# Kernel optimization log

Measured on AMD Instinct MI355X. Metric: run time of the kernel, lower is better.

Reference implementation:

```python
import jax, jax.numpy as jnp
import numpy as np

P, R = 8, 8            # mlp_quad_last_shape: (P, rank)
N, D_IN, HID = 32768, 3, 1024
NQ, QD, QHID = 64, 1, 128


def _mlp2(x, Wa, ba, Wb, bb):
    # two-layer MLP with tanh, matches a standard DecGreenNet MLP block
    return jnp.tanh(x @ Wa + ba) @ Wb + bb


def setup_inputs() -> dict:
    key = jax.random.key(0)
    ks = jax.random.split(key, 32)
    sn = lambda k, shape, scale: (jax.random.normal(k, shape, jnp.float32) * scale)
    inp = {
        "input": jax.random.normal(ks[0], (N, D_IN), jnp.float32),
        "eq_param": jnp.ones((1,), jnp.float32),
        "W1": sn(ks[1], (D_IN, HID), 1.0 / np.sqrt(D_IN)),
        "b1": jnp.zeros((HID,), jnp.float32),
        "W2": sn(ks[2], (HID, P ** 4), 1.0 / np.sqrt(HID)),
        "b2": jnp.zeros((P ** 4,), jnp.float32),
    }
    for i in range(4):
        inp[f"quad_x{i}"] = jax.random.uniform(ks[3 + i], (NQ, QD), jnp.float32)
        inp[f"Wq{i}a"] = sn(ks[7 + 2 * i], (QD, QHID), 1.0)
        inp[f"bq{i}a"] = jnp.zeros((QHID,), jnp.float32)
        inp[f"Wq{i}b"] = sn(ks[8 + 2 * i], (QHID, P * R), 1.0 / np.sqrt(QHID))
        inp[f"bq{i}b"] = jnp.zeros((P * R,), jnp.float32)
    return inp


def reference(input, eq_param, W1, b1, W2, b2,
              quad_x0, quad_x1, quad_x2, quad_x3,
              Wq0a, bq0a, Wq0b, bq0b,
              Wq1a, bq1a, Wq1b, bq1b,
              Wq2a, bq2a, Wq2b, bq2b,
              Wq3a, bq3a, Wq3b, bq3b):
    # lhs = mlp_x(input): [N, P^4]
    lhs = _mlp2(input, W1, b1, W2, b2)

    quads = [(quad_x0, Wq0a, bq0a, Wq0b, bq0b),
             (quad_x1, Wq1a, bq1a, Wq1b, bq1b),
             (quad_x2, Wq2a, bq2a, Wq2b, bq2b),
             (quad_x3, Wq3a, bq3a, Wq3b, bq3b)]

    # Per-factor: y_i * mlp_quad_i(quad_x_i), reshape to [n_i, P, R], sum over quad points.
    # Summing the 8-D outer product over its four quadrature axes factorizes exactly
    # into these per-factor sums S_i followed by a rank contraction (same math as
    # the torch einsum+movedim+reshape+sum, without the (n*P)^4 intermediate).
    Ss = []
    for qx, Wa, ba, Wb, bb in quads:
        y = eq_param * jnp.prod(jnp.sin(jnp.pi * qx), axis=-1, keepdims=True)  # [n,1]
        oq = (y * _mlp2(qx, Wa, ba, Wb, bb)).reshape(-1, P, R)                 # [n,P,R]
        Ss.append(oq.sum(axis=0))                                              # [P,R]

    # rhs[b,d,f,m] = sum_x S0[b,x] S1[d,x] S2[f,x] S3[m,x]; flatten in (b,d,f,m) order
    rhs = jnp.einsum('bx,dx,fx,mx->bdfm', *Ss).reshape(-1)  # [P^4]
    return lhs @ rhs  # [N]
```

## Files before the change

### kernel.cpp

```cpp
#include <hip/hip_runtime.h>
#include <math.h>

#define HID   1024
#define P4    4096

__device__ __forceinline__ float fast_tanh(float x) {
    float e = __expf(-2.0f * fabsf(x));
    float t = (1.0f - e) * __builtin_amdgcn_rcpf(1.0f + e);
    return copysignf(t, x);
}

__global__ __launch_bounds__(256) void k_factors_rhs(
    const float* __restrict__ eq,
    const float* __restrict__ qx0, const float* __restrict__ wa0, const float* __restrict__ ba0,
    const float* __restrict__ wb0, const float* __restrict__ bb0,
    const float* __restrict__ qx1, const float* __restrict__ wa1, const float* __restrict__ ba1,
    const float* __restrict__ wb1, const float* __restrict__ bb1,
    const float* __restrict__ qx2, const float* __restrict__ wa2, const float* __restrict__ ba2,
    const float* __restrict__ wb2, const float* __restrict__ bb2,
    const float* __restrict__ qx3, const float* __restrict__ wa3, const float* __restrict__ ba3,
    const float* __restrict__ wb3, const float* __restrict__ bb3,
    const float* __restrict__ b2,
    float* __restrict__ rhs, float* __restrict__ b2r)
{
    __shared__ float2 qy_s[4][64];
    __shared__ float  wh_s[4][128];
    __shared__ float  S_s[4][64];
    __shared__ float  red[256];

    const int t    = threadIdx.x;
    const int lane = t & 63;
    const int f    = t >> 6;

    const float* qx; const float* wa; const float* ba; const float* wb; const float* bb;
    if (f == 0)      { qx = qx0; wa = wa0; ba = ba0; wb = wb0; bb = bb0; }
    else if (f == 1) { qx = qx1; wa = wa1; ba = ba1; wb = wb1; bb = bb1; }
    else if (f == 2) { qx = qx2; wa = wa2; ba = ba2; wb = wb2; bb = bb2; }
    else             { qx = qx3; wa = wa3; ba = ba3; wb = wb3; bb = bb3; }

    const float qv = qx[lane];
    const float yv = eq[0] * sinf((float)M_PI * qv);
    qy_s[f][lane] = make_float2(qv, yv);

    float ysum = yv;
    #pragma unroll
    for (int off = 32; off; off >>= 1) ysum += __shfl_xor(ysum, off);

    __syncthreads();

    {
        const float w0 = wa[lane],      c0 = ba[lane];
        const float w1 = wa[lane + 64], c1 = ba[lane + 64];
        float a0 = 0.f, a1 = 0.f;
        #pragma unroll 8
        for (int p = 0; p < 64; ++p) {
            float2 qy = qy_s[f][p];
            a0 += qy.y * fast_tanh(fmaf(qy.x, w0, c0));
            a1 += qy.y * fast_tanh(fmaf(qy.x, w1, c1));
        }
        wh_s[f][lane]      = a0;
        wh_s[f][lane + 64] = a1;
    }
    __syncthreads();

    {
        float acc = bb[lane] * ysum;
        #pragma unroll 8
        for (int h = 0; h < 128; ++h)
            acc = fmaf(wh_s[f][h], wb[h * 64 + lane], acc);
        S_s[f][lane] = acc;
    }
    __syncthreads();

    float local = 0.f;
    for (int i = t; i < P4; i += 256) {
        const int m  = i & 7;
        const int fq = (i >> 3) & 7;
        const int d  = (i >> 6) & 7;
        const int b  = (i >> 9) & 7;
        float acc = 0.f;
        #pragma unroll
        for (int x = 0; x < 8; ++x)
            acc += S_s[0][b * 8 + x] * S_s[1][d * 8 + x]
                 * S_s[2][fq * 8 + x] * S_s[3][m * 8 + x];
        rhs[i] = acc;
        local = fmaf(b2[i], acc, local);
    }

    red[t] = local;
    __syncthreads();
    if (t < 128) red[t] += red[t + 128];
    __syncthreads();
    if (t < 64) {
        float v = red[t] + red[t + 64];
        #pragma unroll
        for (int off = 32; off; off >>= 1) v += __shfl_xor(v, off);
        if (t == 0) b2r[0] = v;
    }
}

__global__ __launch_bounds__(256) void k_w2r(
    const float* __restrict__ W2, const float* __restrict__ rhs,
    float* __restrict__ w2r)
{
    const int wave = threadIdx.x >> 6;
    const int lane = threadIdx.x & 63;
    const int row  = blockIdx.x * 4 + wave;

    const float4* w4 = (const float4*)(W2 + (size_t)row * P4);
    const float4* r4 = (const float4*)rhs;

    float acc = 0.f;
    #pragma unroll
    for (int i = 0; i < 16; ++i) {
        const int k = lane + 64 * i;
        float4 a = w4[k];
        float4 b = r4[k];
        acc += a.x * b.x + a.y * b.y + a.z * b.z + a.w * b.w;
    }
    #pragma unroll
    for (int off = 32; off; off >>= 1) acc += __shfl_down(acc, off);
    if (lane == 0) w2r[row] = acc;
}

__global__ __launch_bounds__(256) void k_out(
    const float* __restrict__ input,
    const float* __restrict__ W1, const float* __restrict__ b1,
    const float* __restrict__ w2r, const float* __restrict__ b2r,
    float* __restrict__ out)
{
    __shared__ float4 wpack[HID];
    __shared__ float  w2rs[HID];
    __shared__ float  part[4][64];

    const int t = threadIdx.x;
    #pragma unroll
    for (int h = t; h < HID; h += 256) {
        wpack[h] = make_float4(W1[h], W1[HID + h], W1[2 * HID + h], b1[h]);
        w2rs[h]  = w2r[h];
    }
    __syncthreads();

    const int lane = t & 63;
    const int wave = t >> 6;
    const int row  = blockIdx.x * 64 + lane;
    const float* x = input + (size_t)row * 3;
    const float x0 = x[0], x1 = x[1], x2 = x[2];

    float acc = 0.f;
    const int h0 = wave * 256;
    #pragma unroll 8
    for (int h = h0; h < h0 + 256; ++h) {
        float4 wp = wpack[h];
        float pre = fmaf(x0, wp.x, fmaf(x1, wp.y, fmaf(x2, wp.z, wp.w)));
        acc = fmaf(fast_tanh(pre), w2rs[h], acc);
    }

    part[wave][lane] = acc;
    __syncthreads();
    if (t < 64)
        out[blockIdx.x * 64 + t] =
            part[0][t] + part[1][t] + part[2][t] + part[3][t] + b2r[0];
}

extern "C" void kernel_launch(void* const* d_in, const int* in_sizes, int n_in,
                              void* d_out, int out_size, void* d_ws, size_t ws_size,
                              hipStream_t stream)
{
    const float* input = (const float*)d_in[0];
    const float* eq    = (const float*)d_in[1];
    const float* W1    = (const float*)d_in[2];
    const float* b1    = (const float*)d_in[3];
    const float* W2    = (const float*)d_in[4];
    const float* b2    = (const float*)d_in[5];
    const float* q[4][5];
    for (int i = 0; i < 4; ++i)
        for (int k = 0; k < 5; ++k)
            q[i][k] = (const float*)d_in[6 + 5 * i + k];

    float* ws  = (float*)d_ws;
    float* rhs = ws;
    float* w2r = ws + 4096;
    float* b2r = ws + 5120;
    float* out = (float*)d_out;

    hipLaunchKernelGGL(k_factors_rhs, dim3(1), dim3(256), 0, stream,
        eq,
        q[0][0], q[0][1], q[0][2], q[0][3], q[0][4],
        q[1][0], q[1][1], q[1][2], q[1][3], q[1][4],
        q[2][0], q[2][1], q[2][2], q[2][3], q[2][4],
        q[3][0], q[3][1], q[3][2], q[3][3], q[3][4],
        b2, rhs, b2r);

    hipLaunchKernelGGL(k_w2r, dim3(256), dim3(256), 0, stream,
        W2, rhs, w2r);

    hipLaunchKernelGGL(k_out, dim3(512), dim3(256), 0, stream,
        input, W1, b1, w2r, b2r, out);
}
```

Measured before the change: 143.8 us.

## Fuse three kernels into one cooperative kernel with grid syncs and prefetched W2

Replaces the three launches (factor/rhs, W2·rhs, output MLP) with a single cooperative kernel of 1024 blocks that uses grid.sync between phases. Each block loads its W2 row into registers before the first sync, hiding that load behind the single-block factor computation. Each block then recomputes the full rhs vector in shared memory instead of reading it from global memory. This removes launch gaps and the serialized single-block stage, at the cost of grid-wide barrier overhead, redundant rhs computation, and a requirement that all 1024 blocks be co-resident.

```diff
diff --git a/kernel.cpp b/kernel.cpp
--- a/kernel.cpp
+++ b/kernel.cpp
@@ -1,8 +1,22 @@
 #include <hip/hip_runtime.h>
+#include <hip/hip_cooperative_groups.h>
 #include <math.h>
 
-#define HID   1024
-#define P4    4096
+#define HID 1024
+#define P4  4096
+
+namespace cg = cooperative_groups;
+
+struct Params {
+    const float* input; const float* eq;
+    const float* W1; const float* b1; const float* W2; const float* b2;
+    const float* qx[4]; const float* wa[4]; const float* ba[4];
+    const float* wb[4]; const float* bb[4];
+    float* Sg;
+    float* w2r;
+    float* b2r;
+    float* out;
+};
 
 __device__ __forceinline__ float fast_tanh(float x) {
     float e = __expf(-2.0f * fabsf(x));
@@ -10,70 +24,71 @@
     return copysignf(t, x);
 }
 
-__global__ __launch_bounds__(256) void k_factors_rhs(
-    const float* __restrict__ eq,
-    const float* __restrict__ qx0, const float* __restrict__ wa0, const float* __restrict__ ba0,
-    const float* __restrict__ wb0, const float* __restrict__ bb0,
-    const float* __restrict__ qx1, const float* __restrict__ wa1, const float* __restrict__ ba1,
-    const float* __restrict__ wb1, const float* __restrict__ bb1,
-    const float* __restrict__ qx2, const float* __restrict__ wa2, const float* __restrict__ ba2,
-    const float* __restrict__ wb2, const float* __restrict__ bb2,
-    const float* __restrict__ qx3, const float* __restrict__ wa3, const float* __restrict__ ba3,
-    const float* __restrict__ wb3, const float* __restrict__ bb3,
-    const float* __restrict__ b2,
-    float* __restrict__ rhs, float* __restrict__ b2r)
+__global__ __launch_bounds__(256, 4) void k_fused(Params p)
 {
-    __shared__ float2 qy_s[4][64];
-    __shared__ float  wh_s[4][128];
-    __shared__ float  S_s[4][64];
-    __shared__ float  red[256];
+    union SharedU {
+        struct { float2 qy[64]; float wh[128]; } a;
+        struct { float S[256]; float rhs[P4]; float red[256]; } b;
+        struct { float4 wpack[HID]; float w2rs[HID]; float part[8][32]; } c;
+    };
+    __shared__ SharedU sm;
 
-    const int t    = threadIdx.x;
-    const int lane = t & 63;
-    const int f    = t >> 6;
+    cg::grid_group grid = cg::this_grid();
+    const int bid = blockIdx.x;
+    const int t   = threadIdx.x;
 
-    const float* qx; const float* wa; const float* ba; const float* wb; const float* bb;
-    if (f == 0)      { qx = qx0; wa = wa0; ba = ba0; wb = wb0; bb = bb0; }
-    else if (f == 1) { qx = qx1; wa = wa1; ba = ba1; wb = wb1; bb = bb1; }
-    else if (f == 2) { qx = qx2; wa = wa2; ba = ba2; wb = wb2; bb = bb2; }
-    else             { qx = qx3; wa = wa3; ba = ba3; wb = wb3; bb = bb3; }
+    float4 wreg0, wreg1, wreg2, wreg3;
+    {
+        const float4* w4 = (const float4*)(p.W2 + (size_t)bid * P4);
+        wreg0 = w4[t];
+        wreg1 = w4[t + 256];
+        wreg2 = w4[t + 512];
+        wreg3 = w4[t + 768];
+    }
 
-    const float qv = qx[lane];
-    const float yv = eq[0] * sinf((float)M_PI * qv);
-    qy_s[f][lane] = make_float2(qv, yv);
+    if (bid < 4) {
+        const float* qx = p.qx[bid]; const float* wa = p.wa[bid];
+        const float* ba = p.ba[bid]; const float* wb = p.wb[bid];
+        const float* bb = p.bb[bid];
 
-    float ysum = yv;
-    #pragma unroll
-    for (int off = 32; off; off >>= 1) ysum += __shfl_xor(ysum, off);
+        float ysum = 0.f;
+        if (t < 64) {
+            float qv = qx[t];
+            float yv = p.eq[0] * sinf((float)M_PI * qv);
+            sm.a.qy[t] = make_float2(qv, yv);
+            ysum = yv;
+            #pragma unroll
+            for (int off = 32; off; off >>= 1) ysum += __shfl_xor(ysum, off);
+        }
+        __syncthreads();
+        if (t < 128) {
+            float w = wa[t], c0 = ba[t], a = 0.f;
+            #pragma unroll 8
+            for (int q = 0; q < 64; ++q) {
+                float2 qy = sm.a.qy[q];
+                a += qy.y * fast_tanh(fmaf(qy.x, w, c0));
+            }
+            sm.a.wh[t] = a;
+        }
+        __syncthreads();
+        if (t < 64) {
+            float acc = bb[t] * ysum;
+            #pragma unroll 8
+            for (int h = 0; h < 128; ++h)
+                acc = fmaf(sm.a.wh[h], wb[h * 64 + t], acc);
+            p.Sg[bid * 64 + t] = acc;
+        }
+    }
 
+    grid.sync();
+
+    sm.b.S[t] = p.Sg[t];
     __syncthreads();
 
-    {
-        const float w0 = wa[lane],      c0 = ba[lane];
-        const float w1 = wa[lane + 64], c1 = ba[lane + 64];
-        float a0 = 0.f, a1 = 0.f;
-        #pragma unroll 8
-        for (int p = 0; p < 64; ++p) {
-            float2 qy = qy_s[f][p];
-            a0 += qy.y * fast_tanh(fmaf(qy.x, w0, c0));
-            a1 += qy.y * fast_tanh(fmaf(qy.x, w1, c1));
-        }
-        wh_s[f][lane]      = a0;
-        wh_s[f][lane + 64] = a1;
-    }
-    __syncthreads();
-
-    {
-        float acc = bb[lane] * ysum;
-        #pragma unroll 8
-        for (int h = 0; h < 128; ++h)
-            acc = fmaf(wh_s[f][h], wb[h * 64 + lane], acc);
-        S_s[f][lane] = acc;
-    }
-    __syncthreads();
-
-    float local = 0.f;
-    for (int i = t; i < P4; i += 256) {
+    float b2local = 0.f;
+    #pragma unroll
+    for (int k = 0; k < 16; ++k) {
+        const int i = t + 256 * k;
         const int m  = i & 7;
         const int fq = (i >> 3) & 7;
         const int d  = (i >> 6) & 7;
@@ -81,120 +96,99 @@
         float acc = 0.f;
         #pragma unroll
         for (int x = 0; x < 8; ++x)
-            acc += S_s[0][b * 8 + x] * S_s[1][d * 8 + x]
-                 * S_s[2][fq * 8 + x] * S_s[3][m * 8 + x];
-        rhs[i] = acc;
-        local = fmaf(b2[i], acc, local);
-    }
-
-    red[t] = local;
-    __syncthreads();
-    if (t < 128) red[t] += red[t + 128];
-    __syncthreads();
-    if (t < 64) {
-        float v = red[t] + red[t + 64];
-        #pragma unroll
-        for (int off = 32; off; off >>= 1) v += __shfl_xor(v, off);
-        if (t == 0) b2r[0] = v;
-    }
-}
-
-__global__ __launch_bounds__(256) void k_w2r(
-    const float* __restrict__ W2, const float* __restrict__ rhs,
-    float* __restrict__ w2r)
-{
-    const int wave = threadIdx.x >> 6;
-    const int lane = threadIdx.x & 63;
-    const int row  = blockIdx.x * 4 + wave;
-
-    const float4* w4 = (const float4*)(W2 + (size_t)row * P4);
-    const float4* r4 = (const float4*)rhs;
-
-    float acc = 0.f;
-    #pragma unroll
-    for (int i = 0; i < 16; ++i) {
-        const int k = lane + 64 * i;
-        float4 a = w4[k];
-        float4 b = r4[k];
-        acc += a.x * b.x + a.y * b.y + a.z * b.z + a.w * b.w;
-    }
-    #pragma unroll
-    for (int off = 32; off; off >>= 1) acc += __shfl_down(acc, off);
-    if (lane == 0) w2r[row] = acc;
-}
-
-__global__ __launch_bounds__(256) void k_out(
-    const float* __restrict__ input,
-    const float* __restrict__ W1, const float* __restrict__ b1,
-    const float* __restrict__ w2r, const float* __restrict__ b2r,
-    float* __restrict__ out)
-{
-    __shared__ float4 wpack[HID];
-    __shared__ float  w2rs[HID];
-    __shared__ float  part[4][64];
-
-    const int t = threadIdx.x;
-    #pragma unroll
-    for (int h = t; h < HID; h += 256) {
-        wpack[h] = make_float4(W1[h], W1[HID + h], W1[2 * HID + h], b1[h]);
-        w2rs[h]  = w2r[h];
+            acc += sm.b.S[b * 8 + x]       * sm.b.S[64 + d * 8 + x]
+                 * sm.b.S[128 + fq * 8 + x] * sm.b.S[192 + m * 8 + x];
+        sm.b.rhs[i] = acc;
+        if (bid == 0) b2local = fmaf(p.b2[i], acc, b2local);
     }
     __syncthreads();
 
-    const int lane = t & 63;
-    const int wave = t >> 6;
-    const int row  = blockIdx.x * 64 + lane;
-    const float* x = input + (size_t)row * 3;
+    {
+        const float4* r4 = (const float4*)sm.b.rhs;
+        float4 a0 = r4[t], a1 = r4[t + 256], a2 = r4[t + 512], a3 = r4[t + 768];
+        float acc = wreg0.x * a0.x + wreg0.y * a0.y + wreg0.z * a0.z + wreg0.w * a0.w
+                  + wreg1.x * a1.x + wreg1.y * a1.y + wreg1.z * a1.z + wreg1.w * a1.w
+                  + wreg2.x * a2.x + wreg2.y * a2.y + wreg2.z * a2.z + wreg2.w * a2.w
+                  + wreg3.x * a3.x + wreg3.y * a3.y + wreg3.z * a3.z + wreg3.w * a3.w;
+        sm.b.red[t] = acc;
+    }
+    __syncthreads();
+    if (t < 64) {
+        float v = sm.b.red[t] + sm.b.red[t + 64] + sm.b.red[t + 128] + sm.b.red[t + 192];
+        #pragma unroll
+        for (int off = 32; off; off >>= 1) v += __shfl_xor(v, off);
+        if (t == 0) p.w2r[bid] = v;
+    }
+    if (bid == 0) {
+        __syncthreads();
+        sm.b.red[t] = b2local;
+        __syncthreads();
+        if (t < 64) {
+            float v = sm.b.red[t] + sm.b.red[t + 64] + sm.b.red[t + 128] + sm.b.red[t + 192];
+            #pragma unroll
+            for (int off = 32; off; off >>= 1) v += __shfl_xor(v, off);
+            if (t == 0) p.b2r[0] = v;
+        }
+    }
+
+    grid.sync();
+
+    #pragma unroll
+    for (int h = t; h < HID; h += 256) {
+        sm.c.wpack[h] = make_float4(p.W1[h], p.W1[HID + h], p.W1[2 * HID + h], p.b1[h]);
+        sm.c.w2rs[h]  = p.w2r[h];
+    }
+    __syncthreads();
+
+    const int r = t & 31;
+    const int c = t >> 5;
+    const int row = bid * 32 + r;
+    const float* x = p.input + (size_t)row * 3;
     const float x0 = x[0], x1 = x[1], x2 = x[2];
 
     float acc = 0.f;
-    const int h0 = wave * 256;
+    const int h0 = c * 128;
     #pragma unroll 8
-    for (int h = h0; h < h0 + 256; ++h) {
-        float4 wp = wpack[h];
+    for (int h = h0; h < h0 + 128; ++h) {
+        float4 wp = sm.c.wpack[h];
         float pre = fmaf(x0, wp.x, fmaf(x1, wp.y, fmaf(x2, wp.z, wp.w)));
-        acc = fmaf(fast_tanh(pre), w2rs[h], acc);
+        acc = fmaf(fast_tanh(pre), sm.c.w2rs[h], acc);
     }
-
-    part[wave][lane] = acc;
+    sm.c.part[c][r] = acc;
     __syncthreads();
-    if (t < 64)
-        out[blockIdx.x * 64 + t] =
-            part[0][t] + part[1][t] + part[2][t] + part[3][t] + b2r[0];
+    if (t < 32) {
+        float v = p.b2r[0];
+        #pragma unroll
+        for (int cc = 0; cc < 8; ++cc) v += sm.c.part[cc][t];
+        p.out[bid * 32 + t] = v;
+    }
 }
 
 extern "C" void kernel_launch(void* const* d_in, const int* in_sizes, int n_in,
                               void* d_out, int out_size, void* d_ws, size_t ws_size,
                               hipStream_t stream)
 {
-    const float* input = (const float*)d_in[0];
-    const float* eq    = (const float*)d_in[1];
-    const float* W1    = (const float*)d_in[2];
-    const float* b1    = (const float*)d_in[3];
-    const float* W2    = (const float*)d_in[4];
-    const float* b2    = (const float*)d_in[5];
-    const float* q[4][5];
-    for (int i = 0; i < 4; ++i)
-        for (int k = 0; k < 5; ++k)
-            q[i][k] = (const float*)d_in[6 + 5 * i + k];
+    Params p;
+    p.input = (const float*)d_in[0];
+    p.eq    = (const float*)d_in[1];
+    p.W1    = (const float*)d_in[2];
+    p.b1    = (const float*)d_in[3];
+    p.W2    = (const float*)d_in[4];
+    p.b2    = (const float*)d_in[5];
+    for (int i = 0; i < 4; ++i) {
+        p.qx[i] = (const float*)d_in[6 + 5 * i + 0];
+        p.wa[i] = (const float*)d_in[6 + 5 * i + 1];
+        p.ba[i] = (const float*)d_in[6 + 5 * i + 2];
+        p.wb[i] = (const float*)d_in[6 + 5 * i + 3];
+        p.bb[i] = (const float*)d_in[6 + 5 * i + 4];
+    }
+    float* ws = (float*)d_ws;
+    p.Sg  = ws;
+    p.w2r = ws + 256;
+    p.b2r = ws + 1280;
+    p.out = (float*)d_out;
 
-    float* ws  = (float*)d_ws;
-    float* rhs = ws;
-    float* w2r = ws + 4096;
-    float* b2r = ws + 5120;
-    float* out = (float*)d_out;
-
-    hipLaunchKernelGGL(k_factors_rhs, dim3(1), dim3(256), 0, stream,
-        eq,
-        q[0][0], q[0][1], q[0][2], q[0][3], q[0][4],
-        q[1][0], q[1][1], q[1][2], q[1][3], q[1][4],
-        q[2][0], q[2][1], q[2][2], q[2][3], q[2][4],
-        q[3][0], q[3][1], q[3][2], q[3][3], q[3][4],
-        b2, rhs, b2r);
-
-    hipLaunchKernelGGL(k_w2r, dim3(256), dim3(256), 0, stream,
-        W2, rhs, w2r);
-
-    hipLaunchKernelGGL(k_out, dim3(512), dim3(256), 0, stream,
-        input, W1, b1, w2r, b2r, out);
+    void* args[] = { &p };
+    hipLaunchCooperativeKernel((const void*)k_fused, dim3(1024), dim3(256),
+                               args, 0, stream);
 }
```

Result: slower. 385.1 us (+167.8%).

## Fuse factor computation into W2 reduction and restructure hidden-layer tanh evaluation

Applied to the files above, without the earlier changes.

Merges the single-block factor/rhs kernel with the W2·rhs row reduction. Each of 256 blocks now recomputes the quad MLPs and rhs into shared memory, which removes one launch and the global round trip for rhs. Both kernels rewrite tanh(x) as 1 - 2/(exp(2x)+1) and pull the constant part out algebraically, so each hidden unit costs one exp, one rcp and an FMA. The output kernel now keeps W1 columns in registers per lane, processes 32 rows per block, and reduces across lanes with shuffles. The cost is that the rhs work is repeated in every block, and each output row needs a cross-lane shuffle reduction.

```diff
diff --git a/kernel.cpp b/kernel.cpp
--- a/kernel.cpp
+++ b/kernel.cpp
@@ -1,16 +1,10 @@
 #include <hip/hip_runtime.h>
 #include <math.h>
 
-#define HID   1024
-#define P4    4096
-
-__device__ __forceinline__ float fast_tanh(float x) {
-    float e = __expf(-2.0f * fabsf(x));
-    float t = (1.0f - e) * __builtin_amdgcn_rcpf(1.0f + e);
-    return copysignf(t, x);
-}
-
-__global__ __launch_bounds__(256) void k_factors_rhs(
+#define HID 1024
+#define P4  4096
+
+__global__ __launch_bounds__(256) void k_front(
     const float* __restrict__ eq,
     const float* __restrict__ qx0, const float* __restrict__ wa0, const float* __restrict__ ba0,
     const float* __restrict__ wb0, const float* __restrict__ bb0,
@@ -20,12 +14,13 @@
     const float* __restrict__ wb2, const float* __restrict__ bb2,
     const float* __restrict__ qx3, const float* __restrict__ wa3, const float* __restrict__ ba3,
     const float* __restrict__ wb3, const float* __restrict__ bb3,
-    const float* __restrict__ b2,
-    float* __restrict__ rhs, float* __restrict__ b2r)
+    const float* __restrict__ b2, const float* __restrict__ W2,
+    float* __restrict__ w2r, float* __restrict__ b2r)
 {
-    __shared__ float2 qy_s[4][64];
-    __shared__ float  wh_s[4][128];
-    __shared__ float  S_s[4][64];
+    __shared__ float2 qy[4][64];
+    __shared__ float  wh[4][128];
+    __shared__ float  S[4][64];
+    __shared__ float  rhs_s[P4];
     __shared__ float  red[256];
 
     const int t    = threadIdx.x;
@@ -40,26 +35,26 @@
 
     const float qv = qx[lane];
     const float yv = eq[0] * sinf((float)M_PI * qv);
-    qy_s[f][lane] = make_float2(qv, yv);
-
+    qy[f][lane] = make_float2(qv, yv);
     float ysum = yv;
     #pragma unroll
     for (int off = 32; off; off >>= 1) ysum += __shfl_xor(ysum, off);
-
     __syncthreads();
 
     {
-        const float w0 = wa[lane],      c0 = ba[lane];
-        const float w1 = wa[lane + 64], c1 = ba[lane + 64];
+        const float w0 = 2.f * wa[lane],      c0 = 2.f * ba[lane];
+        const float w1 = 2.f * wa[lane + 64], c1 = 2.f * ba[lane + 64];
         float a0 = 0.f, a1 = 0.f;
         #pragma unroll 8
         for (int p = 0; p < 64; ++p) {
-            float2 qy = qy_s[f][p];
-            a0 += qy.y * fast_tanh(fmaf(qy.x, w0, c0));
-            a1 += qy.y * fast_tanh(fmaf(qy.x, w1, c1));
-        }
-        wh_s[f][lane]      = a0;
-        wh_s[f][lane + 64] = a1;
+            float2 q = qy[f][p];
+            float r0 = __builtin_amdgcn_rcpf(__expf(fmaf(q.x, w0, c0)) + 1.f);
+            float r1 = __builtin_amdgcn_rcpf(__expf(fmaf(q.x, w1, c1)) + 1.f);
+            a0 = fmaf(q.y, r0, a0);
+            a1 = fmaf(q.y, r1, a1);
+        }
+        wh[f][lane]      = ysum - 2.f * a0;
+        wh[f][lane + 64] = ysum - 2.f * a1;
     }
     __syncthreads();
 
@@ -67,60 +62,58 @@
         float acc = bb[lane] * ysum;
         #pragma unroll 8
         for (int h = 0; h < 128; ++h)
-            acc = fmaf(wh_s[f][h], wb[h * 64 + lane], acc);
-        S_s[f][lane] = acc;
-    }
-    __syncthreads();
-
-    float local = 0.f;
-    for (int i = t; i < P4; i += 256) {
+            acc = fmaf(wh[f][h], wb[h * 64 + lane], acc);
+        S[f][lane] = acc;
+    }
+    __syncthreads();
+
+    float ab = 0.f;
+    #pragma unroll
+    for (int k = 0; k < 16; ++k) {
+        const int i  = t + 256 * k;
         const int m  = i & 7;
         const int fq = (i >> 3) & 7;
         const int d  = (i >> 6) & 7;
         const int b  = (i >> 9) & 7;
-        float acc = 0.f;
+        float rv = 0.f;
         #pragma unroll
         for (int x = 0; x < 8; ++x)
-            acc += S_s[0][b * 8 + x] * S_s[1][d * 8 + x]
-                 * S_s[2][fq * 8 + x] * S_s[3][m * 8 + x];
-        rhs[i] = acc;
-        local = fmaf(b2[i], acc, local);
-    }
-
-    red[t] = local;
-    __syncthreads();
-    if (t < 128) red[t] += red[t + 128];
-    __syncthreads();
-    if (t < 64) {
-        float v = red[t] + red[t + 64];
-        #pragma unroll
-        for (int off = 32; off; off >>= 1) v += __shfl_xor(v, off);
-        if (t == 0) b2r[0] = v;
-    }
-}
-
-__global__ __launch_bounds__(256) void k_w2r(
-    const float* __restrict__ W2, const float* __restrict__ rhs,
-    float* __restrict__ w2r)
-{
-    const int wave = threadIdx.x >> 6;
-    const int lane = threadIdx.x & 63;
-    const int row  = blockIdx.x * 4 + wave;
-
-    const float4* w4 = (const float4*)(W2 + (size_t)row * P4);
-    const float4* r4 = (const float4*)rhs;
-
-    float acc = 0.f;
-    #pragma unroll
-    for (int i = 0; i < 16; ++i) {
-        const int k = lane + 64 * i;
-        float4 a = w4[k];
-        float4 b = r4[k];
-        acc += a.x * b.x + a.y * b.y + a.z * b.z + a.w * b.w;
-    }
-    #pragma unroll
-    for (int off = 32; off; off >>= 1) acc += __shfl_down(acc, off);
-    if (lane == 0) w2r[row] = acc;
+            rv += S[0][b * 8 + x] * S[1][d * 8 + x]
+                * S[2][fq * 8 + x] * S[3][m * 8 + x];
+        rhs_s[i] = rv;
+        if (blockIdx.x == 0) ab = fmaf(b2[i], rv, ab);
+    }
+    __syncthreads();
+
+    {
+        const int row = blockIdx.x * 4 + f;
+        const float4* W4 = (const float4*)(W2 + (size_t)row * P4);
+        const float4* R4 = (const float4*)rhs_s;
+        float aw = 0.f;
+        #pragma unroll
+        for (int k = 0; k < 16; ++k) {
+            const int idx = lane + 64 * k;
+            float4 w = W4[idx];
+            float4 r = R4[idx];
+            aw += w.x * r.x + w.y * r.y + w.z * r.z + w.w * r.w;
+        }
+        #pragma unroll
+        for (int off = 32; off; off >>= 1) aw += __shfl_xor(aw, off);
+        if (lane == 0) w2r[row] = aw;
+    }
+
+    if (blockIdx.x == 0) {
+        red[t] = ab;
+        __syncthreads();
+        if (t < 128) red[t] += red[t + 128];
+        __syncthreads();
+        if (t < 64) {
+            float v = red[t] + red[t + 64];
+            #pragma unroll
+            for (int off = 32; off; off >>= 1) v += __shfl_xor(v, off);
+            if (t == 0) b2r[0] = v;
+        }
+    }
 }
 
 __global__ __launch_bounds__(256) void k_out(
@@ -129,38 +122,62 @@
     const float* __restrict__ w2r, const float* __restrict__ b2r,
     float* __restrict__ out)
 {
-    __shared__ float4 wpack[HID];
-    __shared__ float  w2rs[HID];
-    __shared__ float  part[4][64];
-
-    const int t = threadIdx.x;
+    __shared__ float xs[96];
+    __shared__ float part[4][32];
+
+    const int t    = threadIdx.x;
+    const int lane = t & 63;
+    const int w    = t >> 6;
+
+    if (t < 96) xs[t] = input[(size_t)blockIdx.x * 96 + t];
+
+    const int h0 = w * 256 + lane * 4;
+    float4 wa = *(const float4*)(W1 + h0);
+    float4 wb = *(const float4*)(W1 + HID + h0);
+    float4 wc = *(const float4*)(W1 + 2 * HID + h0);
+    float4 bb = *(const float4*)(b1 + h0);
+    float4 wr = *(const float4*)(w2r + h0);
+    wa.x *= 2.f; wa.y *= 2.f; wa.z *= 2.f; wa.w *= 2.f;
+    wb.x *= 2.f; wb.y *= 2.f; wb.z *= 2.f; wb.w *= 2.f;
+    wc.x *= 2.f; wc.y *= 2.f; wc.z *= 2.f; wc.w *= 2.f;
+    bb.x *= 2.f; bb.y *= 2.f; bb.z *= 2.f; bb.w *= 2.f;
+
+    float sw = wr.x + wr.y + wr.z + wr.w;
     #pragma unroll
-    for (int h = t; h < HID; h += 256) {
-        wpack[h] = make_float4(W1[h], W1[HID + h], W1[2 * HID + h], b1[h]);
-        w2rs[h]  = w2r[h];
-    }
-    __syncthreads();
-
-    const int lane = t & 63;
-    const int wave = t >> 6;
-    const int row  = blockIdx.x * 64 + lane;
-    const float* x = input + (size_t)row * 3;
-    const float x0 = x[0], x1 = x[1], x2 = x[2];
-
-    float acc = 0.f;
-    const int h0 = wave * 256;
-    #pragma unroll 8
-    for (int h = h0; h < h0 + 256; ++h) {
-        float4 wp = wpack[h];
-        float pre = fmaf(x0, wp.x, fmaf(x1, wp.y, fmaf(x2, wp.z, wp.w)));
-        acc = fmaf(fast_tanh(pre), w2rs[h], acc);
-    }
-
-    part[wave][lane] = acc;
-    __syncthreads();
-    if (t < 64)
-        out[blockIdx.x * 64 + t] =
-            part[0][t] + part[1][t] + part[2][t] + part[3][t] + b2r[0];
+    for (int off = 32; off; off >>= 1) sw += __shfl_xor(sw, off);
+
+    __syncthreads();
+
+    #pragma unroll 4
+    for (int r = 0; r < 32; ++r) {
+        const float x0 = xs[3 * r + 0];
+        const float x1 = xs[3 * r + 1];
+        const float x2 = xs[3 * r + 2];
+
+        float acc;
+        {
+            float pre0 = fmaf(x2, wc.x, fmaf(x1, wb.x, fmaf(x0, wa.x, bb.x)));
+            float pre1 = fmaf(x2, wc.y, fmaf(x1, wb.y, fmaf(x0, wa.y, bb.y)));
+            float pre2 = fmaf(x2, wc.z, fmaf(x1, wb.z, fmaf(x0, wa.z, bb.z)));
+            float pre3 = fmaf(x2, wc.w, fmaf(x1, wb.w, fmaf(x0, wa.w, bb.w)));
+            float r0 = __builtin_amdgcn_rcpf(__expf(pre0) + 1.f);
+            float r1 = __builtin_amdgcn_rcpf(__expf(pre1) + 1.f);
+            float r2 = __builtin_amdgcn_rcpf(__expf(pre2) + 1.f);
+            float r3 = __builtin_amdgcn_rcpf(__expf(pre3) + 1.f);
+            acc = wr.x * r0;
+            acc = fmaf(wr.y, r1, acc);
+            acc = fmaf(wr.z, r2, acc);
+            acc = fmaf(wr.w, r3, acc);
+        }
+        #pragma unroll
+        for (int off = 32; off; off >>= 1) acc += __shfl_xor(acc, off);
+        if (lane == 0) part[w][r] = sw - 2.f * acc;
+    }
+    __syncthreads();
+
+    if (t < 32)
+        out[(size_t)blockIdx.x * 32 + t] =
+            b2r[0] + part[0][t] + part[1][t] + part[2][t] + part[3][t];
 }
 
 extern "C" void kernel_launch(void* const* d_in, const int* in_sizes, int n_in,
@@ -179,22 +196,18 @@
             q[i][k] = (const float*)d_in[6 + 5 * i + k];
 
     float* ws  = (float*)d_ws;
-    float* rhs = ws;
-    float* w2r = ws + 4096;
-    float* b2r = ws + 5120;
+    float* w2r = ws;
+    float* b2r = ws + 1024;
     float* out = (float*)d_out;
 
-    hipLaunchKernelGGL(k_factors_rhs, dim3(1), dim3(256), 0, stream,
+    hipLaunchKernelGGL(k_front, dim3(256), dim3(256), 0, stream,
         eq,
         q[0][0], q[0][1], q[0][2], q[0][3], q[0][4],
         q[1][0], q[1][1], q[1][2], q[1][3], q[1][4],
         q[2][0], q[2][1], q[2][2], q[2][3], q[2][4],
         q[3][0], q[3][1], q[3][2], q[3][3], q[3][4],
-        b2, rhs, b2r);
-
-    hipLaunchKernelGGL(k_w2r, dim3(256), dim3(256), 0, stream,
-        W2, rhs, w2r);
-
-    hipLaunchKernelGGL(k_out, dim3(512), dim3(256), 0, stream,
+        b2, W2, w2r, b2r);
+
+    hipLaunchKernelGGL(k_out, dim3(1024), dim3(256), 0, stream,
         input, W1, b1, w2r, b2r, out);
 }
```

Measured after the change: 143.0 us. Within noise of the previous version (-0.6%).
